# Kernel tuning notes

Measured on AMD Instinct MI355X. Metric: run time of the kernel, lower is better.

The kernel has to match this reference:

```python
import jax, jax.numpy as jnp
import numpy as np

KS = 3
STRIDE = 1
PADDING = 1
P_SCALE = 10.0
Q_SCALE = 100.0
EPS = 1e-12


def unfold2d(x):
    # x: [N, C, H, W] -> patches [N, C, Hout, Wout, KS*KS]
    x = jnp.pad(x, ((0, 0), (0, 0), (PADDING, PADDING), (PADDING, PADDING)))
    n, c, h, w = x.shape
    hout = (h - KS) // STRIDE + 1
    wout = (w - KS) // STRIDE + 1
    shifts = []
    for a in range(KS):
        for b in range(KS):
            shifts.append(x[:, :, a:a + hout * STRIDE:STRIDE, b:b + wout * STRIDE:STRIDE])
    return jnp.stack(shifts, axis=-1)  # l = a*KS + b, matching flatten of (a, b)


def setup_inputs() -> dict:
    key = jax.random.key(0)
    k1, k2 = jax.random.split(key)
    x = jax.random.normal(k1, (16, 64, 64, 64), dtype=jnp.float32)
    # xavier_uniform for weights [out_c, in_c, k*k]: fan_in=64, fan_out=9 per torch semantics on 3D
    fan_in, fan_out = 64, 9
    limit = float(np.sqrt(6.0 / (fan_in + fan_out)))
    weights = jax.random.uniform(k2, (128, 64, 9), dtype=jnp.float32, minval=-limit, maxval=limit)
    p = jnp.full((128,), float(2 ** 0.5) * P_SCALE, dtype=jnp.float32)
    q = jnp.full((1,), 10.0, dtype=jnp.float32)
    return {"x": x, "weights": weights, "p": p, "q": q}


def reference(x, weights, p, q):
    patches = unfold2d(x)  # [N, C, H, W, L]
    qn = q / Q_SCALE
    scale = jnp.square(qn)  # scalar (shape [1])
    # norm over (C, L) for patches; over (C, L) for weights
    x_norm = jnp.sqrt(jnp.sum(jnp.square(patches), axis=(1, 4), keepdims=True) + EPS) + scale
    w_norm = jnp.sqrt(jnp.sum(jnp.square(weights), axis=(1, 2), keepdims=True) + EPS) + scale
    y = jnp.einsum('nchwl,vcl->nvhw', patches / x_norm, weights / w_norm)
    sign = jnp.sign(y)
    expo = jnp.square(p / P_SCALE)[None, :, None, None]
    return sign * jnp.power(jnp.abs(y) + EPS, expo)
```

## Files before the change

kernel.cpp:

```cpp
#include <hip/hip_runtime.h>
#include <math.h>
#include <stdint.h>

#define EPS 1e-12f

typedef __attribute__((ext_vector_type(8))) short short8v;
typedef __attribute__((ext_vector_type(8))) unsigned short us8;
typedef __attribute__((ext_vector_type(4))) float f32x4;

__device__ __forceinline__ unsigned short f2bf(float f) {
  union { float f; uint32_t u; } c; c.f = f;
  uint32_t u = c.u;
  uint32_t r = (u + 0x7FFFu + ((u >> 16) & 1u)) >> 16;
  return (unsigned short)r;
}


__global__ __launch_bounds__(256) void prep_wb(
    const float* __restrict__ w, const float* __restrict__ q,
    unsigned short* __restrict__ Wb) {
  int tid = threadIdx.x;
  int v = blockIdx.x * 4 + (tid >> 6);
  int c = tid & 63;
  float qn = q[0] * 0.01f;
  float scale = qn * qn;
  const float* wp = w + (v * 64 + c) * 9;
  float vals[9];
  float ss = 0.f;
#pragma unroll
  for (int j = 0; j < 9; ++j) { vals[j] = wp[j]; ss += vals[j] * vals[j]; }
#pragma unroll
  for (int off = 32; off > 0; off >>= 1) ss += __shfl_xor(ss, off);
  float inv = 1.0f / (sqrtf(ss + EPS) + scale);
  int pos = (((c >> 3) ^ (v & 7)) << 3) | (c & 7);
#pragma unroll
  for (int j = 0; j < 9; ++j) Wb[(j * 128 + v) * 64 + pos] = f2bf(vals[j] * inv);
}

__global__ __launch_bounds__(512) void conv_fused(
    const float* __restrict__ x, const unsigned short* __restrict__ Wb,
    const float* __restrict__ p, const float* __restrict__ q,
    float* __restrict__ out) {
  __shared__ unsigned short xs[6 * 66 * 64];
  __shared__ unsigned short wl[128 * 64];
  __shared__ float sf[6 * 64];
  __shared__ float xiv[4 * 64];

  int b = blockIdx.x;
  int n = b >> 4, ht = b & 15;
  int h0 = ht * 4;
  int tid = threadIdx.x;
  int lane = tid & 63, wid = tid >> 6;
  int wv = wid & 1, wp = wid >> 1;
  int lp = lane & 15, lg = lane >> 4;

  const us8* wsrc = (const us8*)Wb + tid;
  us8 wr0 = wsrc[0];
  us8 wr1 = wsrc[512];

  if (wid < 6) {
    int hh = h0 - 1 + wid;
    int w = lane;
    unsigned short* xrow = xs + wid * 4224 + (w + 1) * 64;
    if ((unsigned)hh < 64u) {
      const float* xp = x + ((size_t)n << 18) + hh * 64 + w;
      float ss = 0.f;
#pragma unroll
      for (int j = 0; j < 8; ++j) {
        float v[8];
#pragma unroll
        for (int e = 0; e < 8; ++e) v[e] = xp[(j * 8 + e) * 4096];
        us8 pk;
#pragma unroll
        for (int e = 0; e < 8; ++e) { ss += v[e] * v[e]; pk[e] = f2bf(v[e]); }
        *(us8*)(xrow + ((j ^ (w & 7)) * 8)) = pk;
      }
      sf[wid * 64 + w] = ss;
    } else {
      us8 z = {};
#pragma unroll
      for (int j = 0; j < 8; ++j) *(us8*)(xrow + j * 8) = z;
      sf[wid * 64 + w] = 0.f;
    }
  } else {
    int t = tid - 384;
    if (t < 96) {
      int row = t >> 4, side = (t >> 3) & 1, j = t & 7;
      us8 z = {};
      *(us8*)(xs + row * 4224 + (side ? 65 : 0) * 64 + j * 8) = z;
    }
  }
  us8* wl8 = (us8*)wl;
  wl8[tid] = wr0;
  wl8[tid + 512] = wr1;
  __syncthreads();

  if (tid < 256) {
    int r = tid >> 6, w = tid & 63;
    float qn = q[0] * 0.01f;
    float scale = qn * qn;
    float a = 0.f;
#pragma unroll
    for (int dr = 0; dr < 3; ++dr) {
      const float* base = sf + (r + dr) * 64;
      a += base[w];
      if (w > 0) a += base[w - 1];
      if (w < 63) a += base[w + 1];
    }
    xiv[r * 64 + w] = 1.0f / (sqrtf(a + EPS) + scale);
  }

  f32x4 acc[4][4];
#pragma unroll
  for (int i = 0; i < 4; ++i)
#pragma unroll
    for (int j = 0; j < 4; ++j) acc[i][j] = (f32x4){0.f, 0.f, 0.f, 0.f};

  const unsigned short* wbase = wl + wv * 4096;

#pragma unroll
  for (int l = 0; l < 9; ++l) {
    us8 nw0 = {}, nw1 = {};
    if (l < 8) {
      nw0 = wsrc[(l + 1) * 1024];
      nw1 = wsrc[(l + 1) * 1024 + 512];
    }
    const int a = l / 3, bs = l % 3;
    const unsigned short* xrow = xs + (wp + a) * 4224;
#pragma unroll
    for (int half = 0; half < 2; ++half) {
      const int cbase = half * 4;
      short8v av[4], bv[4];
#pragma unroll
      for (int vg = 0; vg < 4; ++vg)
        av[vg] = *(const short8v*)(wbase + (vg * 16 + lp) * 64 +
                                   ((cbase + lg) ^ (lp & 7)) * 8);
#pragma unroll
      for (int pg = 0; pg < 4; ++pg) {
        int wx = pg * 16 + lp + bs - 1;
        bv[pg] = *(const short8v*)(xrow + (wx + 1) * 64 +
                                   ((cbase + lg) ^ (wx & 7)) * 8);
      }
#pragma unroll
      for (int pg = 0; pg < 4; ++pg)
#pragma unroll
        for (int vg = 0; vg < 4; ++vg)
          acc[pg][vg] = __builtin_amdgcn_mfma_f32_16x16x32_bf16(
              bv[pg], av[vg], acc[pg][vg], 0, 0, 0);
    }
    if (l < 8) {
      __syncthreads();
      wl8[tid] = nw0;
      wl8[tid + 512] = nw1;
      __syncthreads();
    }
  }

  int h = h0 + wp;
#pragma unroll
  for (int vg = 0; vg < 4; ++vg) {
    int v = wv * 64 + vg * 16 + lp;
    float t0 = p[v] * 0.1f;
    float e = t0 * t0;
    float* ob = out + ((size_t)(n * 128 + v)) * 4096 + h * 64;
#pragma unroll
    for (int pg = 0; pg < 4; ++pg) {
      int w4 = pg * 16 + lg * 4;
      float4 xv = *(const float4*)&xiv[wp * 64 + w4];
      float yv[4] = {acc[pg][vg][0] * xv.x, acc[pg][vg][1] * xv.y,
                     acc[pg][vg][2] * xv.z, acc[pg][vg][3] * xv.w};
      float4 o;
      float* ov = (float*)&o;
#pragma unroll
      for (int r = 0; r < 4; ++r) {
        float y = yv[r];
        float t = fabsf(y) + EPS;
        float rv = exp2f(e * log2f(t));
        ov[r] = (y == 0.0f) ? 0.0f : copysignf(rv, y);
      }
      *(float4*)(ob + w4) = o;
    }
  }
}

extern "C" void kernel_launch(void* const* d_in, const int* in_sizes, int n_in,
                              void* d_out, int out_size, void* d_ws, size_t ws_size,
                              hipStream_t stream) {
  const float* x = (const float*)d_in[0];
  const float* w = (const float*)d_in[1];
  const float* p = (const float*)d_in[2];
  const float* q = (const float*)d_in[3];
  float* out = (float*)d_out;

  unsigned short* Wb = (unsigned short*)d_ws;

  prep_wb<<<32, 256, 0, stream>>>(w, q, Wb);
  conv_fused<<<256, 512, 0, stream>>>(x, Wb, p, q, out);
}
```

Baseline: 29.64 us.

## Halve row tile, double-buffer weights via direct global-to-LDS loads

Each block now handles 2 output rows with 256 threads, and 512 blocks are launched with launch bounds targeting 2 blocks per CU. Weight slices for each kernel tap are staged straight into a double-buffered LDS region with global_load_lds, which drops the register round-trip and one barrier per tap. Output is written with nontemporal stores. The cost is more redundant loading and normalization of halo input rows per output row (4 input rows for 2 output rows instead of 6 for 4), plus extra LDS for the second weight buffer.

```diff
diff --git a/kernel.cpp b/kernel.cpp
--- a/kernel.cpp
+++ b/kernel.cpp
@@ -13,6 +13,12 @@
   uint32_t u = c.u;
   uint32_t r = (u + 0x7FFFu + ((u >> 16) & 1u)) >> 16;
   return (unsigned short)r;
+}
+
+__device__ __forceinline__ void gl_lds16(const void* g, void* l) {
+  __builtin_amdgcn_global_load_lds(
+      (const __attribute__((address_space(1))) unsigned int*)g,
+      (__attribute__((address_space(3))) unsigned int*)l, 16, 0, 0);
 }
 
 
@@ -37,28 +43,33 @@
   for (int j = 0; j < 9; ++j) Wb[(j * 128 + v) * 64 + pos] = f2bf(vals[j] * inv);
 }
 
-__global__ __launch_bounds__(512) void conv_fused(
+__global__ __launch_bounds__(256, 2) void conv_fused(
     const float* __restrict__ x, const unsigned short* __restrict__ Wb,
     const float* __restrict__ p, const float* __restrict__ q,
     float* __restrict__ out) {
-  __shared__ unsigned short xs[6 * 66 * 64];
-  __shared__ unsigned short wl[128 * 64];
-  __shared__ float sf[6 * 64];
-  __shared__ float xiv[4 * 64];
+  __shared__ unsigned short xs[4 * 66 * 64];
+  __shared__ unsigned short wl[2 * 128 * 64];
+  __shared__ float sf[4 * 64];
+  __shared__ float xiv[2 * 64];
 
   int b = blockIdx.x;
-  int n = b >> 4, ht = b & 15;
-  int h0 = ht * 4;
+  int n = b >> 5, hg = b & 31;
+  int h0 = hg * 2;
   int tid = threadIdx.x;
   int lane = tid & 63, wid = tid >> 6;
   int wv = wid & 1, wp = wid >> 1;
   int lp = lane & 15, lg = lane >> 4;
 
-  const us8* wsrc = (const us8*)Wb + tid;
-  us8 wr0 = wsrc[0];
-  us8 wr1 = wsrc[512];
+  auto stage_w = [&](int bufi, int l) {
+    const unsigned short* src = Wb + l * 8192 + wid * 2048;
+    unsigned short* dst = wl + bufi * 8192 + wid * 2048;
+#pragma unroll
+    for (int i = 0; i < 4; ++i)
+      gl_lds16(src + i * 512 + lane * 8, dst + i * 512);
+  };
+  stage_w(0, 0);
 
-  if (wid < 6) {
+  {
     int hh = h0 - 1 + wid;
     int w = lane;
     unsigned short* xrow = xs + wid * 4224 + (w + 1) * 64;
@@ -82,20 +93,15 @@
       for (int j = 0; j < 8; ++j) *(us8*)(xrow + j * 8) = z;
       sf[wid * 64 + w] = 0.f;
     }
-  } else {
-    int t = tid - 384;
-    if (t < 96) {
-      int row = t >> 4, side = (t >> 3) & 1, j = t & 7;
-      us8 z = {};
-      *(us8*)(xs + row * 4224 + (side ? 65 : 0) * 64 + j * 8) = z;
-    }
   }
-  us8* wl8 = (us8*)wl;
-  wl8[tid] = wr0;
-  wl8[tid + 512] = wr1;
+  if (tid < 64) {
+    int row = tid >> 4, side = (tid >> 3) & 1, j = tid & 7;
+    us8 z = {};
+    *(us8*)(xs + row * 4224 + (side ? 65 : 0) * 64 + j * 8) = z;
+  }
   __syncthreads();
 
-  if (tid < 256) {
+  if (tid < 128) {
     int r = tid >> 6, w = tid & 63;
     float qn = q[0] * 0.01f;
     float scale = qn * qn;
@@ -116,17 +122,13 @@
 #pragma unroll
     for (int j = 0; j < 4; ++j) acc[i][j] = (f32x4){0.f, 0.f, 0.f, 0.f};
 
-  const unsigned short* wbase = wl + wv * 4096;
-
+  int buf = 0;
 #pragma unroll
   for (int l = 0; l < 9; ++l) {
-    us8 nw0 = {}, nw1 = {};
-    if (l < 8) {
-      nw0 = wsrc[(l + 1) * 1024];
-      nw1 = wsrc[(l + 1) * 1024 + 512];
-    }
+    if (l < 8) stage_w(buf ^ 1, l + 1);
     const int a = l / 3, bs = l % 3;
     const unsigned short* xrow = xs + (wp + a) * 4224;
+    const unsigned short* wbase = wl + buf * 8192 + wv * 4096;
 #pragma unroll
     for (int half = 0; half < 2; ++half) {
       const int cbase = half * 4;
@@ -150,9 +152,7 @@
     }
     if (l < 8) {
       __syncthreads();
-      wl8[tid] = nw0;
-      wl8[tid + 512] = nw1;
-      __syncthreads();
+      buf ^= 1;
     }
   }
 
@@ -169,16 +169,15 @@
       float4 xv = *(const float4*)&xiv[wp * 64 + w4];
       float yv[4] = {acc[pg][vg][0] * xv.x, acc[pg][vg][1] * xv.y,
                      acc[pg][vg][2] * xv.z, acc[pg][vg][3] * xv.w};
-      float4 o;
-      float* ov = (float*)&o;
+      f32x4 o;
 #pragma unroll
       for (int r = 0; r < 4; ++r) {
         float y = yv[r];
         float t = fabsf(y) + EPS;
         float rv = exp2f(e * log2f(t));
-        ov[r] = (y == 0.0f) ? 0.0f : copysignf(rv, y);
+        o[r] = (y == 0.0f) ? 0.0f : copysignf(rv, y);
       }
-      *(float4*)(ob + w4) = o;
+      __builtin_nontemporal_store(o, (f32x4*)(ob + w4));
     }
   }
 }
@@ -195,5 +194,5 @@
   unsigned short* Wb = (unsigned short*)d_ws;
 
   prep_wb<<<32, 256, 0, stream>>>(w, q, Wb);
-  conv_fused<<<256, 512, 0, stream>>>(x, Wb, p, q, out);
+  conv_fused<<<512, 256, 0, stream>>>(x, Wb, p, q, out);
 }
```

Result: slower. 30.27 us (+2.1%).
